# Optimization experiments

Hardware: AMD Instinct MI355X
Metric: run time of the kernel (lower is better)

## Reference

```python
import jax, jax.numpy as jnp
import numpy as np

VOCAB, D_MODEL, NHEAD, NLAYER, DIM_FF, MAX_LEN = 32000, 1024, 16, 6, 4096, 1024
B, L = 8, 1024
PAD_ID = 0
EPS = 1e-5


def _ln(x, g, b):
    m = x.mean(-1, keepdims=True)
    v = x.var(-1, keepdims=True)
    return (x - m) / jnp.sqrt(v + EPS) * g + b


def _mha(x, Wqkv, bqkv, Wo, bo, kpm):
    # x: [B,L,D]; Wqkv: [3D,D]; kpm: [B,L] bool (True = padded key)
    Bx, Lx, D = x.shape
    dh = D // NHEAD
    qkv = x @ Wqkv.T + bqkv                       # [B,L,3D]
    q, k, v = jnp.split(qkv, 3, axis=-1)
    sp = lambda t: t.reshape(Bx, Lx, NHEAD, dh).transpose(0, 2, 1, 3)  # [B,H,L,dh]
    q, k, v = sp(q), sp(k), sp(v)
    scores = jnp.einsum('bhqd,bhkd->bhqk', q, k) * (dh ** -0.5)
    scores = jnp.where(kpm[:, None, None, :], jnp.asarray(-1e9, scores.dtype), scores)
    attn = jax.nn.softmax(scores, axis=-1)        # explicit weights, as ForceWeightsMHA demands
    o = jnp.einsum('bhqk,bhkd->bhqd', attn, v)
    o = o.transpose(0, 2, 1, 3).reshape(Bx, Lx, D)
    return o @ Wo.T + bo


def setup_inputs() -> dict:
    key = jax.random.key(0)
    ks = jax.random.split(key, 20)
    s = 0.02
    n = lambda k, shp: (jax.random.normal(k, shp, dtype=jnp.float32) * s)
    inp = {
        'input_ids': jax.random.randint(ks[0], (B, L), 0, VOCAB, dtype=jnp.int64) if jax.config.jax_enable_x64 else jax.random.randint(ks[0], (B, L), 0, VOCAB).astype(jnp.int32),
        'tok_emb': n(ks[1], (VOCAB, D_MODEL)),
        'pos_emb': n(ks[2], (MAX_LEN, D_MODEL)),
        'Wqkv': n(ks[3], (NLAYER, 3 * D_MODEL, D_MODEL)),
        'bqkv': jnp.zeros((NLAYER, 3 * D_MODEL), jnp.float32),
        'Wo': n(ks[4], (NLAYER, D_MODEL, D_MODEL)),
        'bo': jnp.zeros((NLAYER, D_MODEL), jnp.float32),
        'ln1_g': jnp.ones((NLAYER, D_MODEL), jnp.float32),
        'ln1_b': jnp.zeros((NLAYER, D_MODEL), jnp.float32),
        'W1': n(ks[5], (NLAYER, DIM_FF, D_MODEL)),
        'b1': jnp.zeros((NLAYER, DIM_FF), jnp.float32),
        'W2': n(ks[6], (NLAYER, D_MODEL, DIM_FF)),
        'b2': jnp.zeros((NLAYER, D_MODEL), jnp.float32),
        'ln2_g': jnp.ones((NLAYER, D_MODEL), jnp.float32),
        'ln2_b': jnp.zeros((NLAYER, D_MODEL), jnp.float32),
        'head_ln_g': jnp.ones((D_MODEL,), jnp.float32),
        'head_ln_b': jnp.zeros((D_MODEL,), jnp.float32),
        'head_W': n(ks[7], (MAX_LEN, D_MODEL)),
        'head_b': jnp.zeros((MAX_LEN,), jnp.float32),
    }
    return inp


def reference(input_ids, tok_emb, pos_emb, Wqkv, bqkv, Wo, bo, ln1_g, ln1_b,
              W1, b1, W2, b2, ln2_g, ln2_b, head_ln_g, head_ln_b, head_W, head_b):
    Bx, Lx = input_ids.shape
    x = tok_emb[input_ids] + pos_emb[None, :Lx]           # [B,L,D]
    kpm = (input_ids == PAD_ID).at[:, 0].set(False)        # key padding mask, col 0 forced valid
    for i in range(NLAYER):                                # post-norm encoder layer (PyTorch default)
        x = _ln(x + _mha(x, Wqkv[i], bqkv[i], Wo[i], bo[i], kpm), ln1_g[i], ln1_b[i])
        ff = jax.nn.gelu(x @ W1[i].T + b1[i], approximate=False) @ W2[i].T + b2[i]
        x = _ln(x + ff, ln2_g[i], ln2_b[i])
    cls = x[:, 0, :]                                       # [B,D]
    return _ln(cls, head_ln_g, head_ln_b) @ head_W.T + head_b  # [B,MAX_LEN]
```

## Files before the change

kernel.cpp:

```cpp
#include <hip/hip_runtime.h>
#include <cstdint>

#define D_MODEL 1024
#define NHEAD   16
#define NLAYER  6
#define DIM_FF  4096
#define SEQ_B   8
#define SEQ_L   1024
#define TOKENS  (SEQ_B*SEQ_L)

typedef __bf16 v8bf  __attribute__((ext_vector_type(8)));
typedef __bf16 v4bf  __attribute__((ext_vector_type(4)));
typedef float  v4f   __attribute__((ext_vector_type(4)));

__device__ __forceinline__ void gl_lds16(const void* g, void* l) {
  __builtin_amdgcn_global_load_lds(
      (const __attribute__((address_space(1))) void*)g,
      (__attribute__((address_space(3))) void*)l, 16, 0, 0);
}

__global__ __launch_bounds__(256) void f2b_kernel(const float4* __restrict__ in,
                                                  ushort4* __restrict__ out, long n4) {
  long i = (long)blockIdx.x * 256 + threadIdx.x;
  long stride = (long)gridDim.x * 256;
  for (; i < n4; i += stride) {
    float4 v = in[i];
    v4bf r = { (__bf16)v.x, (__bf16)v.y, (__bf16)v.z, (__bf16)v.w };
    out[i] = *(ushort4*)&r;
  }
}

__global__ __launch_bounds__(256) void embed_kernel(const int* __restrict__ ids,
    const float4* __restrict__ tok, const float4* __restrict__ pos,
    float4* __restrict__ X, ushort4* __restrict__ Xb) {
  long i = (long)blockIdx.x * 256 + threadIdx.x;
  int d4 = (int)(i & 255);
  long bl = i >> 8;
  int l = (int)(bl & (SEQ_L - 1));
  int id = ids[bl];
  float4 t = tok[(long)id * 256 + d4];
  float4 p = pos[(long)l * 256 + d4];
  float4 v = {t.x + p.x, t.y + p.y, t.z + p.z, t.w + p.w};
  X[i] = v;
  v4bf r = { (__bf16)v.x, (__bf16)v.y, (__bf16)v.z, (__bf16)v.w };
  Xb[i] = *(ushort4*)&r;
}

__global__ __launch_bounds__(256) void maskb_kernel(const int* __restrict__ ids,
                                                    float* __restrict__ mb) {
  int i = blockIdx.x * 256 + threadIdx.x;
  mb[i] = (ids[i] == 0 && (i & 1023) != 0) ? -1e9f : 0.f;
}

template<int EPI>
__global__ __launch_bounds__(256) void gemm128(
    const unsigned short* __restrict__ A,
    const unsigned short* __restrict__ W,
    const float* __restrict__ bias,
    float* __restrict__ Cf, unsigned short* __restrict__ Cb,
    unsigned short* __restrict__ Vt,
    int M, int N, int K) {
  __shared__ unsigned short As[128 * 32];
  __shared__ unsigned short Bs[128 * 32];
  int tid = threadIdx.x;
  int wave = tid >> 6, lane = tid & 63;
  int l15 = lane & 15, quad = lane >> 4;

  int id = blockIdx.y * gridDim.x + blockIdx.x;
  int xcd = id & 7, sidx = id >> 3;
  int mt = xcd * 8 + (sidx & 7);
  int nt = sidx >> 3;
  int m0 = mt * 128, n0 = nt * 128;
  int wm = (wave >> 1) * 64, wn = (wave & 1) * 64;

  int srow = tid >> 2;
  int ssl  = (tid & 3) ^ ((srow >> 1) & 3);
  int sc8  = ssl << 3;
  const unsigned short* Ag0 = A + (long)(m0 + srow) * K + sc8;
  const unsigned short* Ag1 = A + (long)(m0 + srow + 64) * K + sc8;
  const unsigned short* Wg0 = W + (long)(n0 + srow) * K + sc8;
  const unsigned short* Wg1 = W + (long)(n0 + srow + 64) * K + sc8;
  unsigned short* As0 = As + tid * 8;
  unsigned short* As1 = As + tid * 8 + 2048;
  unsigned short* Bs0 = Bs + tid * 8;
  unsigned short* Bs1 = Bs + tid * 8 + 2048;

  const unsigned short* afp[4];
  const unsigned short* bfp[4];
  #pragma unroll
  for (int i = 0; i < 4; ++i) {
    int r = wm + i * 16 + l15;
    afp[i] = &As[r * 32 + ((quad ^ ((r >> 1) & 3)) << 3)];
    int rb = wn + i * 16 + l15;
    bfp[i] = &Bs[rb * 32 + ((quad ^ ((rb >> 1) & 3)) << 3)];
  }

  v4f acc[4][4];
  #pragma unroll
  for (int i = 0; i < 4; ++i)
    #pragma unroll
    for (int j = 0; j < 4; ++j) acc[i][j] = (v4f){0.f, 0.f, 0.f, 0.f};

  int ksteps = K >> 5;
  for (int ks = 0; ks < ksteps; ++ks) {
    int k0 = ks << 5;
    __syncthreads();
    gl_lds16(Ag0 + k0, As0);
    gl_lds16(Ag1 + k0, As1);
    gl_lds16(Wg0 + k0, Bs0);
    gl_lds16(Wg1 + k0, Bs1);
    __syncthreads();
    v8bf af[4], bf[4];
    #pragma unroll
    for (int i = 0; i < 4; ++i) af[i] = *(const v8bf*)afp[i];
    #pragma unroll
    for (int j = 0; j < 4; ++j) bf[j] = *(const v8bf*)bfp[j];
    #pragma unroll
    for (int i = 0; i < 4; ++i)
      #pragma unroll
      for (int j = 0; j < 4; ++j)
        acc[i][j] = __builtin_amdgcn_mfma_f32_16x16x32_bf16(af[i], bf[j], acc[i][j], 0, 0, 0);
  }

  #pragma unroll
  for (int i = 0; i < 4; ++i) {
    int crow0 = m0 + wm + i * 16 + quad * 4;
    #pragma unroll
    for (int j = 0; j < 4; ++j) {
      int col = n0 + wn + j * 16 + l15;
      float bv = bias[col];
      if (EPI == 3 && col >= 2048) {
        int hc = (col - 2048) >> 6, d = (col - 2048) & 63;
        int bb = crow0 >> 10, l = crow0 & 1023;
        v4bf pk = { (__bf16)(acc[i][j][0] + bv), (__bf16)(acc[i][j][1] + bv),
                    (__bf16)(acc[i][j][2] + bv), (__bf16)(acc[i][j][3] + bv) };
        *(ushort4*)&Vt[((long)((bb * 16 + hc) * 64 + d)) * 1024 + l] = *(ushort4*)&pk;
      } else {
        #pragma unroll
        for (int r = 0; r < 4; ++r) {
          float v = acc[i][j][r] + bv;
          if (EPI == 1) v = 0.5f * v * (1.f + erff(v * 0.70710678118f));
          long idx = (long)(crow0 + r) * N + col;
          if (EPI == 0) Cf[idx] = v;
          else          ((__bf16*)Cb)[idx] = (__bf16)v;
        }
      }
    }
  }
}

#define PSP 72
__global__ __launch_bounds__(256) void attn2(
    const unsigned short* __restrict__ QKVb,
    const unsigned short* __restrict__ Vtg,
    const float* __restrict__ mb,
    unsigned short* __restrict__ Ob) {
  __shared__ unsigned short Ks[64 * 64];
  __shared__ unsigned short Vs[64 * 64];
  __shared__ unsigned short Ps[4][16 * PSP];
  int tid = threadIdx.x, wave = tid >> 6, lane = tid & 63;
  int l15 = lane & 15, quad = lane >> 4;
  int b = blockIdx.z, h = blockIdx.y, q0 = blockIdx.x * 64;

  int qrow = q0 + wave * 16 + l15;
  const unsigned short* qb = QKVb + (long)(b * 1024 + qrow) * 3072 + h * 64;
  v8bf gq0 = *(const v8bf*)(qb + quad * 8);
  v8bf gq1 = *(const v8bf*)(qb + 32 + quad * 8);

  v8bf bones;
  #pragma unroll
  for (int j = 0; j < 8; ++j) bones[j] = (l15 == 0) ? (__bf16)1.0f : (__bf16)0.0f;

  float m_run[4], l_run[4];
  v4f O[4];
  #pragma unroll
  for (int r = 0; r < 4; ++r) { m_run[r] = -1e30f; l_run[r] = 0.f; }
  #pragma unroll
  for (int j = 0; j < 4; ++j) O[j] = (v4f){0.f, 0.f, 0.f, 0.f};

  const unsigned short* kgb = QKVb + (long)b * 1024 * 3072 + 1024 + h * 64;
  const unsigned short* vgb = Vtg + (long)((b * 16 + h) * 64) * 1024;
  const float* mrow = mb + b * 1024;

  int srow = tid >> 3;
  int ssl  = (tid & 7) ^ (srow & 7);
  int ph0 = (quad ^ (l15 & 7)) << 3;
  int ph1 = ((quad + 4) ^ (l15 & 7)) << 3;
  const float SC = 0.18033688011112042f;

  for (int k0 = 0; k0 < SEQ_L; k0 += 64) {
    __syncthreads();
    gl_lds16(kgb + (long)(k0 + srow) * 3072 + ssl * 8, &Ks[tid * 8]);
    gl_lds16(kgb + (long)(k0 + srow + 32) * 3072 + ssl * 8, &Ks[tid * 8 + 2048]);
    gl_lds16(vgb + (long)srow * 1024 + k0 + ssl * 8, &Vs[tid * 8]);
    gl_lds16(vgb + (long)(srow + 32) * 1024 + k0 + ssl * 8, &Vs[tid * 8 + 2048]);
    __syncthreads();

    float p[4][4], mr[4];
    #pragma unroll
    for (int r = 0; r < 4; ++r) mr[r] = -1e30f;
    #pragma unroll
    for (int t = 0; t < 4; ++t) {
      int kr = t * 16 + l15;
      v8bf kf0 = *(const v8bf*)&Ks[kr * 64 + ph0];
      v8bf kf1 = *(const v8bf*)&Ks[kr * 64 + ph1];
      v4f s = (v4f){0.f, 0.f, 0.f, 0.f};
      s = __builtin_amdgcn_mfma_f32_16x16x32_bf16(gq0, kf0, s, 0, 0, 0);
      s = __builtin_amdgcn_mfma_f32_16x16x32_bf16(gq1, kf1, s, 0, 0, 0);
      float bv = mrow[k0 + kr];
      #pragma unroll
      for (int r = 0; r < 4; ++r) {
        float sv = fmaf(s[r], SC, bv);
        p[t][r] = sv;
        mr[r] = fmaxf(mr[r], sv);
      }
    }
    #pragma unroll
    for (int r = 0; r < 4; ++r) {
      mr[r] = fmaxf(mr[r], __shfl_xor(mr[r], 1, 64));
      mr[r] = fmaxf(mr[r], __shfl_xor(mr[r], 2, 64));
      mr[r] = fmaxf(mr[r], __shfl_xor(mr[r], 4, 64));
      mr[r] = fmaxf(mr[r], __shfl_xor(mr[r], 8, 64));
    }
    float alpha[4];
    #pragma unroll
    for (int r = 0; r < 4; ++r) {
      float mn = fmaxf(m_run[r], mr[r]);
      alpha[r] = __builtin_amdgcn_exp2f(m_run[r] - mn);
      m_run[r] = mn;
    }
    #pragma unroll
    for (int t = 0; t < 4; ++t)
      #pragma unroll
      for (int r = 0; r < 4; ++r)
        p[t][r] = __builtin_amdgcn_exp2f(p[t][r] - m_run[r]);

    #pragma unroll
    for (int t = 0; t < 4; ++t)
      #pragma unroll
      for (int r = 0; r < 4; ++r)
        ((__bf16*)Ps[wave])[(quad * 4 + r) * PSP + t * 16 + l15] = (__bf16)p[t][r];
    v8bf pa0 = *(const v8bf*)&Ps[wave][l15 * PSP + quad * 8];
    v8bf pa1 = *(const v8bf*)&Ps[wave][l15 * PSP + 32 + quad * 8];

    v4f ss = (v4f){0.f, 0.f, 0.f, 0.f};
    ss = __builtin_amdgcn_mfma_f32_16x16x32_bf16(pa0, bones, ss, 0, 0, 0);
    ss = __builtin_amdgcn_mfma_f32_16x16x32_bf16(pa1, bones, ss, 0, 0, 0);

    #pragma unroll
    for (int j = 0; j < 4; ++j)
      #pragma unroll
      for (int r = 0; r < 4; ++r) O[j][r] *= alpha[r];
    #pragma unroll
    for (int j = 0; j < 4; ++j) {
      v8bf vf0 = *(const v8bf*)&Vs[(j * 16 + l15) * 64 + ph0];
      v8bf vf1 = *(const v8bf*)&Vs[(j * 16 + l15) * 64 + ph1];
      O[j] = __builtin_amdgcn_mfma_f32_16x16x32_bf16(pa0, vf0, O[j], 0, 0, 0);
      O[j] = __builtin_amdgcn_mfma_f32_16x16x32_bf16(pa1, vf1, O[j], 0, 0, 0);
    }
    #pragma unroll
    for (int r = 0; r < 4; ++r)
      l_run[r] = l_run[r] * alpha[r] + __shfl(ss[r], quad << 4, 64);
  }

  int qd = q0 + wave * 16 + quad * 4;
  #pragma unroll
  for (int r = 0; r < 4; ++r) {
    float inv = 1.f / l_run[r];
    #pragma unroll
    for (int j = 0; j < 4; ++j)
      ((__bf16*)Ob)[(long)(b * 1024 + qd + r) * 1024 + h * 64 + j * 16 + l15] =
          (__bf16)(O[j][r] * inv);
  }
}

__global__ __launch_bounds__(256) void add_ln(
    const float* __restrict__ Xin, const float* __restrict__ Yin,
    const float* __restrict__ g, const float* __restrict__ bta,
    float* __restrict__ outF, unsigned short* __restrict__ outB,
    long in_stride, long out_stride) {
  int row = blockIdx.x;
  const float* x = Xin + (long)row * in_stride;
  const float* y = Yin ? Yin + (long)row * 1024 : nullptr;
  int tid = threadIdx.x;
  float v[4];
  float s = 0.f, s2 = 0.f;
  #pragma unroll
  for (int j = 0; j < 4; ++j) {
    int d = j * 256 + tid;
    float t = x[d] + (y ? y[d] : 0.f);
    v[j] = t; s += t; s2 += t * t;
  }
  __shared__ float red[8];
  int lane = tid & 63, wave = tid >> 6;
  #pragma unroll
  for (int o = 32; o > 0; o >>= 1) { s += __shfl_down(s, o, 64); s2 += __shfl_down(s2, o, 64); }
  if (lane == 0) { red[wave] = s; red[4 + wave] = s2; }
  __syncthreads();
  s  = red[0] + red[1] + red[2] + red[3];
  s2 = red[4] + red[5] + red[6] + red[7];
  float mean = s * (1.f / 1024.f);
  float var  = s2 * (1.f / 1024.f) - mean * mean;
  float rstd = rsqrtf(var + 1e-5f);
  float* of = outF + (long)row * out_stride;
  unsigned short* ob = outB ? outB + (long)row * out_stride : nullptr;
  #pragma unroll
  for (int j = 0; j < 4; ++j) {
    int d = j * 256 + tid;
    float o = (v[j] - mean) * rstd * g[d] + bta[d];
    of[d] = o;
    if (ob) ((__bf16*)ob)[d] = (__bf16)o;
  }
}

__global__ __launch_bounds__(256) void head_kernel(
    const float* __restrict__ cls, const float* __restrict__ hW,
    const float* __restrict__ hb, float* __restrict__ out) {
  int n = blockIdx.x * 256 + threadIdx.x;
  int b = blockIdx.y;
  const float4* c4 = (const float4*)(cls + b * 1024);
  const float4* w4 = (const float4*)(hW + (long)n * 1024);
  float s = 0.f;
  #pragma unroll 8
  for (int d = 0; d < 256; ++d) {
    float4 a = c4[d], w = w4[d];
    s += a.x * w.x + a.y * w.y + a.z * w.z + a.w * w.w;
  }
  out[b * 1024 + n] = s + hb[n];
}

extern "C" void kernel_launch(void* const* d_in, const int* in_sizes, int n_in,
                              void* d_out, int out_size, void* d_ws, size_t ws_size,
                              hipStream_t stream) {
  const int*   ids  = (const int*)d_in[0];
  const float* tok  = (const float*)d_in[1];
  const float* pos  = (const float*)d_in[2];
  const float* Wqkv = (const float*)d_in[3];
  const float* bqkv = (const float*)d_in[4];
  const float* Wo   = (const float*)d_in[5];
  const float* bo   = (const float*)d_in[6];
  const float* ln1g = (const float*)d_in[7];
  const float* ln1b = (const float*)d_in[8];
  const float* W1   = (const float*)d_in[9];
  const float* b1   = (const float*)d_in[10];
  const float* W2   = (const float*)d_in[11];
  const float* b2   = (const float*)d_in[12];
  const float* ln2g = (const float*)d_in[13];
  const float* ln2b = (const float*)d_in[14];
  const float* hlng = (const float*)d_in[15];
  const float* hlnb = (const float*)d_in[16];
  const float* hW   = (const float*)d_in[17];
  const float* hb   = (const float*)d_in[18];
  float* out = (float*)d_out;

  char* ws = (char*)d_ws;
  size_t off = 0;
  auto alloc = [&](size_t bytes) {
    char* p = ws + off;
    off = (off + bytes + 255) & ~(size_t)255;
    return p;
  };
  unsigned short* Wqkv_b = (unsigned short*)alloc((size_t)NLAYER*3072*1024*2);
  unsigned short* Wo_b   = (unsigned short*)alloc((size_t)NLAYER*1024*1024*2);
  unsigned short* W1_b   = (unsigned short*)alloc((size_t)NLAYER*4096*1024*2);
  unsigned short* W2_b   = (unsigned short*)alloc((size_t)NLAYER*1024*4096*2);
  float*          X      = (float*)alloc((size_t)TOKENS*1024*4);
  unsigned short* Xb     = (unsigned short*)alloc((size_t)TOKENS*1024*2);
  unsigned short* Qb     = (unsigned short*)alloc((size_t)TOKENS*3072*2);
  unsigned short* Vtg    = (unsigned short*)alloc((size_t)TOKENS*1024*2);
  float*          Y      = (float*)alloc((size_t)TOKENS*1024*4);
  unsigned short* Ab     = (unsigned short*)alloc((size_t)TOKENS*1024*2);
  unsigned short* Gb     = Qb;
  float*          cls    = (float*)alloc(8*1024*4);
  float*          mb     = (float*)alloc(TOKENS*4);

  f2b_kernel<<<2048, 256, 0, stream>>>((const float4*)Wqkv, (ushort4*)Wqkv_b, (long)NLAYER*3072*1024/4);
  f2b_kernel<<<2048, 256, 0, stream>>>((const float4*)Wo,   (ushort4*)Wo_b,   (long)NLAYER*1024*1024/4);
  f2b_kernel<<<2048, 256, 0, stream>>>((const float4*)W1,   (ushort4*)W1_b,   (long)NLAYER*4096*1024/4);
  f2b_kernel<<<2048, 256, 0, stream>>>((const float4*)W2,   (ushort4*)W2_b,   (long)NLAYER*1024*4096/4);
  embed_kernel<<<(TOKENS*256)/256, 256, 0, stream>>>(ids, (const float4*)tok, (const float4*)pos,
                                                     (float4*)X, (ushort4*)Xb);
  maskb_kernel<<<TOKENS/256, 256, 0, stream>>>(ids, mb);

  for (int i = 0; i < NLAYER; ++i) {
    gemm128<3><<<dim3(3072/128, TOKENS/128), 256, 0, stream>>>(
        Xb, Wqkv_b + (size_t)i*3072*1024, bqkv + i*3072, nullptr, Qb, Vtg, TOKENS, 3072, 1024);
    attn2<<<dim3(SEQ_L/64, NHEAD, SEQ_B), 256, 0, stream>>>(Qb, Vtg, mb, Ab);
    gemm128<0><<<dim3(1024/128, TOKENS/128), 256, 0, stream>>>(
        Ab, Wo_b + (size_t)i*1024*1024, bo + i*1024, Y, nullptr, nullptr, TOKENS, 1024, 1024);
    add_ln<<<TOKENS, 256, 0, stream>>>(X, Y, ln1g + i*1024, ln1b + i*1024, X, Xb, 1024L, 1024L);
    gemm128<1><<<dim3(4096/128, TOKENS/128), 256, 0, stream>>>(
        Xb, W1_b + (size_t)i*4096*1024, b1 + i*4096, nullptr, Gb, nullptr, TOKENS, 4096, 1024);
    gemm128<0><<<dim3(1024/128, TOKENS/128), 256, 0, stream>>>(
        Gb, W2_b + (size_t)i*1024*4096, b2 + i*1024, Y, nullptr, nullptr, TOKENS, 1024, 4096);
    add_ln<<<TOKENS, 256, 0, stream>>>(X, Y, ln2g + i*1024, ln2b + i*1024, X, Xb, 1024L, 1024L);
  }
  add_ln<<<8, 256, 0, stream>>>(X, nullptr, hlng, hlnb, cls, nullptr, (long)SEQ_L*1024, 1024L);
  head_kernel<<<dim3(4, 8), 256, 0, stream>>>(cls, hW, hb, out);
}
```

Before: 3.351 ms.

## Double-buffer GEMM and attention tiles, fuse residual add, use tanh GELU

Adds LDS double buffering to the bf16 GEMM and to the attention K/V tiles so global-to-LDS loads overlap MFMA work. The attention block now covers 128 queries per block, reusing each K/V tile across two query sub-tiles. The residual add moves into the GEMM epilogue, and the erf GELU is replaced by a tanh approximation built on exp2. This raises register and LDS use, and the GELU approximation changes numerics slightly.

Measured after the change: 3.402 ms. About the same (+1.5%).

```diff
diff --git a/kernel.cpp b/kernel.cpp
--- a/kernel.cpp
+++ b/kernel.cpp
@@ -57,11 +57,12 @@
     const unsigned short* __restrict__ A,
     const unsigned short* __restrict__ W,
     const float* __restrict__ bias,
+    const float* __restrict__ Res,
     float* __restrict__ Cf, unsigned short* __restrict__ Cb,
     unsigned short* __restrict__ Vt,
     int M, int N, int K) {
-  __shared__ unsigned short As[128 * 32];
-  __shared__ unsigned short Bs[128 * 32];
+  __shared__ unsigned short As[2 * 128 * 32];
+  __shared__ unsigned short Bs[2 * 128 * 32];
   int tid = threadIdx.x;
   int wave = tid >> 6, lane = tid & 63;
   int l15 = lane & 15, quad = lane >> 4;
@@ -81,9 +82,7 @@
   const unsigned short* Wg0 = W + (long)(n0 + srow) * K + sc8;
   const unsigned short* Wg1 = W + (long)(n0 + srow + 64) * K + sc8;
   unsigned short* As0 = As + tid * 8;
-  unsigned short* As1 = As + tid * 8 + 2048;
   unsigned short* Bs0 = Bs + tid * 8;
-  unsigned short* Bs1 = Bs + tid * 8 + 2048;
 
   const unsigned short* afp[4];
   const unsigned short* bfp[4];
@@ -101,25 +100,44 @@
     #pragma unroll
     for (int j = 0; j < 4; ++j) acc[i][j] = (v4f){0.f, 0.f, 0.f, 0.f};
 
+  auto compute = [&](int bo) {
+    v8bf af[4], bb[4];
+    #pragma unroll
+    for (int i = 0; i < 4; ++i) af[i] = *(const v8bf*)(afp[i] + bo);
+    #pragma unroll
+    for (int j = 0; j < 4; ++j) bb[j] = *(const v8bf*)(bfp[j] + bo);
+    #pragma unroll
+    for (int i = 0; i < 4; ++i)
+      #pragma unroll
+      for (int j = 0; j < 4; ++j)
+        acc[i][j] = __builtin_amdgcn_mfma_f32_16x16x32_bf16(af[i], bb[j], acc[i][j], 0, 0, 0);
+  };
+
+  gl_lds16(Ag0, As0);
+  gl_lds16(Ag1, As0 + 2048);
+  gl_lds16(Wg0, Bs0);
+  gl_lds16(Wg1, Bs0 + 2048);
+
   int ksteps = K >> 5;
-  for (int ks = 0; ks < ksteps; ++ks) {
-    int k0 = ks << 5;
+  for (int ks = 0; ks < ksteps; ks += 2) {
     __syncthreads();
-    gl_lds16(Ag0 + k0, As0);
-    gl_lds16(Ag1 + k0, As1);
-    gl_lds16(Wg0 + k0, Bs0);
-    gl_lds16(Wg1 + k0, Bs1);
+    {
+      int k1 = (ks + 1) << 5;
+      gl_lds16(Ag0 + k1, As0 + 4096);
+      gl_lds16(Ag1 + k1, As0 + 6144);
+      gl_lds16(Wg0 + k1, Bs0 + 4096);
+      gl_lds16(Wg1 + k1, Bs0 + 6144);
+    }
+    compute(0);
     __syncthreads();
-    v8bf af[4], bf[4];
-    #pragma unroll
-    for (int i = 0; i < 4; ++i) af[i] = *(const v8bf*)afp[i];
-    #pragma unroll
-    for (int j = 0; j < 4; ++j) bf[j] = *(const v8bf*)bfp[j];
-    #pragma unroll
-    for (int i = 0; i < 4; ++i)
-      #pragma unroll
-      for (int j = 0; j < 4; ++j)
-        acc[i][j] = __builtin_amdgcn_mfma_f32_16x16x32_bf16(af[i], bf[j], acc[i][j], 0, 0, 0);
+    if (ks + 2 < ksteps) {
+      int k2 = (ks + 2) << 5;
+      gl_lds16(Ag0 + k2, As0);
+      gl_lds16(Ag1 + k2, As0 + 2048);
+      gl_lds16(Wg0 + k2, Bs0);
+      gl_lds16(Wg1 + k2, Bs0 + 2048);
+    }
+    compute(4096);
   }
 
   #pragma unroll
@@ -131,17 +149,22 @@
       float bv = bias[col];
       if (EPI == 3 && col >= 2048) {
         int hc = (col - 2048) >> 6, d = (col - 2048) & 63;
-        int bb = crow0 >> 10, l = crow0 & 1023;
+        int bb2 = crow0 >> 10, l = crow0 & 1023;
         v4bf pk = { (__bf16)(acc[i][j][0] + bv), (__bf16)(acc[i][j][1] + bv),
                     (__bf16)(acc[i][j][2] + bv), (__bf16)(acc[i][j][3] + bv) };
-        *(ushort4*)&Vt[((long)((bb * 16 + hc) * 64 + d)) * 1024 + l] = *(ushort4*)&pk;
+        *(ushort4*)&Vt[((long)((bb2 * 16 + hc) * 64 + d)) * 1024 + l] = *(ushort4*)&pk;
       } else {
         #pragma unroll
         for (int r = 0; r < 4; ++r) {
           float v = acc[i][j][r] + bv;
-          if (EPI == 1) v = 0.5f * v * (1.f + erff(v * 0.70710678118f));
           long idx = (long)(crow0 + r) * N + col;
-          if (EPI == 0) Cf[idx] = v;
+          if (EPI == 1) {
+            float u = v * (0.7978845608028654f + 0.03567740814f * v * v);
+            float e = __builtin_amdgcn_exp2f(u * 2.885390081777927f);
+            float th = 1.f - 2.f / (e + 1.f);
+            v = 0.5f * v * (1.f + th);
+          }
+          if (EPI == 0) Cf[idx] = v + Res[idx];
           else          ((__bf16*)Cb)[idx] = (__bf16)v;
         }
       }
@@ -155,28 +178,35 @@
     const unsigned short* __restrict__ Vtg,
     const float* __restrict__ mb,
     unsigned short* __restrict__ Ob) {
-  __shared__ unsigned short Ks[64 * 64];
-  __shared__ unsigned short Vs[64 * 64];
+  __shared__ unsigned short Ks[2 * 64 * 64];
+  __shared__ unsigned short Vs[2 * 64 * 64];
   __shared__ unsigned short Ps[4][16 * PSP];
   int tid = threadIdx.x, wave = tid >> 6, lane = tid & 63;
   int l15 = lane & 15, quad = lane >> 4;
-  int b = blockIdx.z, h = blockIdx.y, q0 = blockIdx.x * 64;
-
-  int qrow = q0 + wave * 16 + l15;
-  const unsigned short* qb = QKVb + (long)(b * 1024 + qrow) * 3072 + h * 64;
-  v8bf gq0 = *(const v8bf*)(qb + quad * 8);
-  v8bf gq1 = *(const v8bf*)(qb + 32 + quad * 8);
+  int b = blockIdx.z, h = blockIdx.y, q0 = blockIdx.x * 128;
+
+  v8bf gq[2][2];
+  #pragma unroll
+  for (int t = 0; t < 2; ++t) {
+    int qrow = q0 + t * 64 + wave * 16 + l15;
+    const unsigned short* qb = QKVb + (long)(b * 1024 + qrow) * 3072 + h * 64;
+    gq[t][0] = *(const v8bf*)(qb + quad * 8);
+    gq[t][1] = *(const v8bf*)(qb + 32 + quad * 8);
+  }
 
   v8bf bones;
   #pragma unroll
   for (int j = 0; j < 8; ++j) bones[j] = (l15 == 0) ? (__bf16)1.0f : (__bf16)0.0f;
 
-  float m_run[4], l_run[4];
-  v4f O[4];
-  #pragma unroll
-  for (int r = 0; r < 4; ++r) { m_run[r] = -1e30f; l_run[r] = 0.f; }
-  #pragma unroll
-  for (int j = 0; j < 4; ++j) O[j] = (v4f){0.f, 0.f, 0.f, 0.f};
+  float m_run[2][4], l_run[2][4];
+  v4f O[2][4];
+  #pragma unroll
+  for (int t = 0; t < 2; ++t)
+    #pragma unroll
+    for (int r = 0; r < 4; ++r) {
+      m_run[t][r] = -1e30f; l_run[t][r] = 0.f;
+      O[t][r] = (v4f){0.f, 0.f, 0.f, 0.f};
+    }
 
   const unsigned short* kgb = QKVb + (long)b * 1024 * 3072 + 1024 + h * 64;
   const unsigned short* vgb = Vtg + (long)((b * 16 + h) * 64) * 1024;
@@ -188,89 +218,116 @@
   int ph1 = ((quad + 4) ^ (l15 & 7)) << 3;
   const float SC = 0.18033688011112042f;
 
-  for (int k0 = 0; k0 < SEQ_L; k0 += 64) {
+  gl_lds16(kgb + (long)srow * 3072 + ssl * 8, &Ks[tid * 8]);
+  gl_lds16(kgb + (long)(srow + 32) * 3072 + ssl * 8, &Ks[tid * 8 + 2048]);
+  gl_lds16(vgb + (long)srow * 1024 + ssl * 8, &Vs[tid * 8]);
+  gl_lds16(vgb + (long)(srow + 32) * 1024 + ssl * 8, &Vs[tid * 8 + 2048]);
+
+  for (int c = 0; c < 16; ++c) {
+    int cbo = (c & 1) * 4096;
     __syncthreads();
-    gl_lds16(kgb + (long)(k0 + srow) * 3072 + ssl * 8, &Ks[tid * 8]);
-    gl_lds16(kgb + (long)(k0 + srow + 32) * 3072 + ssl * 8, &Ks[tid * 8 + 2048]);
-    gl_lds16(vgb + (long)srow * 1024 + k0 + ssl * 8, &Vs[tid * 8]);
-    gl_lds16(vgb + (long)(srow + 32) * 1024 + k0 + ssl * 8, &Vs[tid * 8 + 2048]);
-    __syncthreads();
-
-    float p[4][4], mr[4];
-    #pragma unroll
-    for (int r = 0; r < 4; ++r) mr[r] = -1e30f;
+    if (c + 1 < 16) {
+      int nbo = 4096 - cbo;
+      int k0n = (c + 1) * 64;
+      gl_lds16(kgb + (long)(k0n + srow) * 3072 + ssl * 8, &Ks[nbo + tid * 8]);
+      gl_lds16(kgb + (long)(k0n + srow + 32) * 3072 + ssl * 8, &Ks[nbo + tid * 8 + 2048]);
+      gl_lds16(vgb + (long)srow * 1024 + k0n + ssl * 8, &Vs[nbo + tid * 8]);
+      gl_lds16(vgb + (long)(srow + 32) * 1024 + k0n + ssl * 8, &Vs[nbo + tid * 8 + 2048]);
+    }
+    int k0 = c * 64;
+
+    v8bf kf0[4], kf1[4];
     #pragma unroll
     for (int t = 0; t < 4; ++t) {
-      int kr = t * 16 + l15;
-      v8bf kf0 = *(const v8bf*)&Ks[kr * 64 + ph0];
-      v8bf kf1 = *(const v8bf*)&Ks[kr * 64 + ph1];
-      v4f s = (v4f){0.f, 0.f, 0.f, 0.f};
-      s = __builtin_amdgcn_mfma_f32_16x16x32_bf16(gq0, kf0, s, 0, 0, 0);
-      s = __builtin_amdgcn_mfma_f32_16x16x32_bf16(gq1, kf1, s, 0, 0, 0);
-      float bv = mrow[k0 + kr];
+      kf0[t] = *(const v8bf*)&Ks[cbo + (t * 16 + l15) * 64 + ph0];
+      kf1[t] = *(const v8bf*)&Ks[cbo + (t * 16 + l15) * 64 + ph1];
+    }
+    float mbv[4];
+    #pragma unroll
+    for (int t = 0; t < 4; ++t) mbv[t] = mrow[k0 + t * 16 + l15];
+
+    #pragma unroll
+    for (int tt = 0; tt < 2; ++tt) {
+      float p[4][4], mr[4];
+      #pragma unroll
+      for (int r = 0; r < 4; ++r) mr[r] = -1e30f;
+      #pragma unroll
+      for (int t = 0; t < 4; ++t) {
+        v4f s = (v4f){0.f, 0.f, 0.f, 0.f};
+        s = __builtin_amdgcn_mfma_f32_16x16x32_bf16(gq[tt][0], kf0[t], s, 0, 0, 0);
+        s = __builtin_amdgcn_mfma_f32_16x16x32_bf16(gq[tt][1], kf1[t], s, 0, 0, 0);
+        #pragma unroll
+        for (int r = 0; r < 4; ++r) {
+          float sv = fmaf(s[r], SC, mbv[t]);
+          p[t][r] = sv;
+          mr[r] = fmaxf(mr[r], sv);
+        }
+      }
       #pragma unroll
       for (int r = 0; r < 4; ++r) {
-        float sv = fmaf(s[r], SC, bv);
-        p[t][r] = sv;
-        mr[r] = fmaxf(mr[r], sv);
+        mr[r] = fmaxf(mr[r], __shfl_xor(mr[r], 1, 64));
+        mr[r] = fmaxf(mr[r], __shfl_xor(mr[r], 2, 64));
+        mr[r] = fmaxf(mr[r], __shfl_xor(mr[r], 4, 64));
+        mr[r] = fmaxf(mr[r], __shfl_xor(mr[r], 8, 64));
       }
-    }
+      float alpha[4];
+      #pragma unroll
+      for (int r = 0; r < 4; ++r) {
+        float mn = fmaxf(m_run[tt][r], mr[r]);
+        alpha[r] = __builtin_amdgcn_exp2f(m_run[tt][r] - mn);
+        m_run[tt][r] = mn;
+      }
+      #pragma unroll
+      for (int t = 0; t < 4; ++t)
+        #pragma unroll
+        for (int r = 0; r < 4; ++r)
+          p[t][r] = __builtin_amdgcn_exp2f(p[t][r] - m_run[tt][r]);
+
+      #pragma unroll
+      for (int t = 0; t < 4; ++t)
+        #pragma unroll
+        for (int r = 0; r < 4; ++r)
+          ((__bf16*)Ps[wave])[(quad * 4 + r) * PSP + t * 16 + l15] = (__bf16)p[t][r];
+      v8bf pa0 = *(const v8bf*)&Ps[wave][l15 * PSP + quad * 8];
+      v8bf pa1 = *(const v8bf*)&Ps[wave][l15 * PSP + 32 + quad * 8];
+
+      v4f ss = (v4f){0.f, 0.f, 0.f, 0.f};
+      ss = __builtin_amdgcn_mfma_f32_16x16x32_bf16(pa0, bones, ss, 0, 0, 0);
+      ss = __builtin_amdgcn_mfma_f32_16x16x32_bf16(pa1, bones, ss, 0, 0, 0);
+
+      #pragma unroll
+      for (int j = 0; j < 4; ++j)
+        #pragma unroll
+        for (int r = 0; r < 4; ++r) O[tt][j >= 0 ? j : j][r] *= (j == 0 ? alpha[r] : 1.f);
+      #pragma unroll
+      for (int j = 1; j < 4; ++j)
+        #pragma unroll
+        for (int r = 0; r < 4; ++r) O[tt][j][r] *= alpha[r];
+
+      #pragma unroll
+      for (int j = 0; j < 4; ++j) {
+        v8bf vf0 = *(const v8bf*)&Vs[cbo + (j * 16 + l15) * 64 + ph0];
+        v8bf vf1 = *(const v8bf*)&Vs[cbo + (j * 16 + l15) * 64 + ph1];
+        O[tt][j] = __builtin_amdgcn_mfma_f32_16x16x32_bf16(pa0, vf0, O[tt][j], 0, 0, 0);
+        O[tt][j] = __builtin_amdgcn_mfma_f32_16x16x32_bf16(pa1, vf1, O[tt][j], 0, 0, 0);
+      }
+      #pragma unroll
+      for (int r = 0; r < 4; ++r)
+        l_run[tt][r] = l_run[tt][r] * alpha[r] + __shfl(ss[r], quad << 4, 64);
+    }
+  }
+
+  #pragma unroll
+  for (int tt = 0; tt < 2; ++tt) {
+    int qd = q0 + tt * 64 + wave * 16 + quad * 4;
     #pragma unroll
     for (int r = 0; r < 4; ++r) {
-      mr[r] = fmaxf(mr[r], __shfl_xor(mr[r], 1, 64));
-      mr[r] = fmaxf(mr[r], __shfl_xor(mr[r], 2, 64));
-      mr[r] = fmaxf(mr[r], __shfl_xor(mr[r], 4, 64));
-      mr[r] = fmaxf(mr[r], __shfl_xor(mr[r], 8, 64));
-    }
-    float alpha[4];
-    #pragma unroll
-    for (int r = 0; r < 4; ++r) {
-      float mn = fmaxf(m_run[r], mr[r]);
-      alpha[r] = __builtin_amdgcn_exp2f(m_run[r] - mn);
-      m_run[r] = mn;
-    }
-    #pragma unroll
-    for (int t = 0; t < 4; ++t)
-      #pragma unroll
-      for (int r = 0; r < 4; ++r)
-        p[t][r] = __builtin_amdgcn_exp2f(p[t][r] - m_run[r]);
-
-    #pragma unroll
-    for (int t = 0; t < 4; ++t)
-      #pragma unroll
-      for (int r = 0; r < 4; ++r)
-        ((__bf16*)Ps[wave])[(quad * 4 + r) * PSP + t * 16 + l15] = (__bf16)p[t][r];
-    v8bf pa0 = *(const v8bf*)&Ps[wave][l15 * PSP + quad * 8];
-    v8bf pa1 = *(const v8bf*)&Ps[wave][l15 * PSP + 32 + quad * 8];
-
-    v4f ss = (v4f){0.f, 0.f, 0.f, 0.f};
-    ss = __builtin_amdgcn_mfma_f32_16x16x32_bf16(pa0, bones, ss, 0, 0, 0);
-    ss = __builtin_amdgcn_mfma_f32_16x16x32_bf16(pa1, bones, ss, 0, 0, 0);
-
-    #pragma unroll
-    for (int j = 0; j < 4; ++j)
-      #pragma unroll
-      for (int r = 0; r < 4; ++r) O[j][r] *= alpha[r];
-    #pragma unroll
-    for (int j = 0; j < 4; ++j) {
-      v8bf vf0 = *(const v8bf*)&Vs[(j * 16 + l15) * 64 + ph0];
-      v8bf vf1 = *(const v8bf*)&Vs[(j * 16 + l15) * 64 + ph1];
-      O[j] = __builtin_amdgcn_mfma_f32_16x16x32_bf16(pa0, vf0, O[j], 0, 0, 0);
-      O[j] = __builtin_amdgcn_mfma_f32_16x16x32_bf16(pa1, vf1, O[j], 0, 0, 0);
-    }
-    #pragma unroll
-    for (int r = 0; r < 4; ++r)
-      l_run[r] = l_run[r] * alpha[r] + __shfl(ss[r], quad << 4, 64);
-  }
-
-  int qd = q0 + wave * 16 + quad * 4;
-  #pragma unroll
-  for (int r = 0; r < 4; ++r) {
-    float inv = 1.f / l_run[r];
-    #pragma unroll
-    for (int j = 0; j < 4; ++j)
-      ((__bf16*)Ob)[(long)(b * 1024 + qd + r) * 1024 + h * 64 + j * 16 + l15] =
-          (__bf16)(O[j][r] * inv);
+      float inv = 1.f / l_run[tt][r];
+      #pragma unroll
+      for (int j = 0; j < 4; ++j)
+        ((__bf16*)Ob)[(long)(b * 1024 + qd + r) * 1024 + h * 64 + j * 16 + l15] =
+            (__bf16)(O[tt][j][r] * inv);
+    }
   }
 }
 
@@ -384,16 +441,16 @@
 
   for (int i = 0; i < NLAYER; ++i) {
     gemm128<3><<<dim3(3072/128, TOKENS/128), 256, 0, stream>>>(
-        Xb, Wqkv_b + (size_t)i*3072*1024, bqkv + i*3072, nullptr, Qb, Vtg, TOKENS, 3072, 1024);
-    attn2<<<dim3(SEQ_L/64, NHEAD, SEQ_B), 256, 0, stream>>>(Qb, Vtg, mb, Ab);
+        Xb, Wqkv_b + (size_t)i*3072*1024, bqkv + i*3072, nullptr, nullptr, Qb, Vtg, TOKENS, 3072, 1024);
+    attn2<<<dim3(SEQ_L/128, NHEAD, SEQ_B), 256, 0, stream>>>(Qb, Vtg, mb, Ab);
     gemm128<0><<<dim3(1024/128, TOKENS/128), 256, 0, stream>>>(
-        Ab, Wo_b + (size_t)i*1024*1024, bo + i*1024, Y, nullptr, nullptr, TOKENS, 1024, 1024);
-    add_ln<<<TOKENS, 256, 0, stream>>>(X, Y, ln1g + i*1024, ln1b + i*1024, X, Xb, 1024L, 1024L);
+        Ab, Wo_b + (size_t)i*1024*1024, bo + i*1024, X, Y, nullptr, nullptr, TOKENS, 1024, 1024);
+    add_ln<<<TOKENS, 256, 0, stream>>>(Y, nullptr, ln1g + i*1024, ln1b + i*1024, X, Xb, 1024L, 1024L);
     gemm128<1><<<dim3(4096/128, TOKENS/128), 256, 0, stream>>>(
-        Xb, W1_b + (size_t)i*4096*1024, b1 + i*4096, nullptr, Gb, nullptr, TOKENS, 4096, 1024);
+        Xb, W1_b + (size_t)i*4096*1024, b1 + i*4096, nullptr, nullptr, Gb, nullptr, TOKENS, 4096, 1024);
     gemm128<0><<<dim3(1024/128, TOKENS/128), 256, 0, stream>>>(
-        Gb, W2_b + (size_t)i*1024*4096, b2 + i*1024, Y, nullptr, nullptr, TOKENS, 1024, 4096);
-    add_ln<<<TOKENS, 256, 0, stream>>>(X, Y, ln2g + i*1024, ln2b + i*1024, X, Xb, 1024L, 1024L);
+        Gb, W2_b + (size_t)i*1024*4096, b2 + i*1024, X, Y, nullptr, nullptr, TOKENS, 1024, 4096);
+    add_ln<<<TOKENS, 256, 0, stream>>>(Y, nullptr, ln2g + i*1024, ln2b + i*1024, X, Xb, 1024L, 1024L);
   }
   add_ln<<<8, 256, 0, stream>>>(X, nullptr, hlng, hlnb, cls, nullptr, (long)SEQ_L*1024, 1024L);
   head_kernel<<<dim3(4, 8), 256, 0, stream>>>(cls, hW, hb, out);
```
